# Kernel tuning notes

Measured on AMD Instinct MI355X. Metric: run time of the kernel, lower is better.

## Reference

```python
import jax, jax.numpy as jnp
from jax import lax
import numpy as np

T_NO = 50       # history / kernel half-length (hard-coded in module)
T_MAX = 101     # basis kernel length = 2*T_NO + 1
BASIS_NO = 34
HIST_BASIS_NO = 18
SIGMA = 3.0
HID = 20
SUB = 20


def _make_basis(n_basis, length):
    # basis[i, t] = exp(-(t - 3*i)^2 / sigma)
    raw = jnp.arange(length, dtype=jnp.float32)
    pts = 3.0 * jnp.arange(n_basis, dtype=jnp.float32)
    return jnp.exp(-((raw[None, :] - pts[:, None]) ** 2) / SIGMA)


def _conv1d(x, kern, pad):
    # x: [1, Cin, T], kern: [Cout, Cin, K] -> [1, Cout, T'] (torch F.conv1d semantics, cross-correlation)
    return lax.conv_general_dilated(x, kern, window_strides=(1,), padding=[(pad, pad)],
                                    dimension_numbers=('NCH', 'OIH', 'NCH'))


def setup_inputs() -> dict:
    key = jax.random.key(0)
    ks = jax.random.split(key, 12)
    T, Ee, Ei = 200000, 500, 100
    S_e = (jax.random.uniform(ks[0], (T, Ee)) < 0.05).astype(jnp.float32)
    S_i = (jax.random.uniform(ks[1], (T, Ei)) < 0.05).astype(jnp.float32)
    # one-hot synapse->subunit connectivity, as in the original model
    C_syn_e = jax.nn.one_hot(jax.random.randint(ks[2], (Ee,), 0, SUB), SUB, dtype=jnp.float32).T
    C_syn_i = jax.nn.one_hot(jax.random.randint(ks[3], (Ei,), 0, SUB), SUB, dtype=jnp.float32).T
    weight1 = 0.01 * jax.random.normal(ks[4], (HID, 2 * SUB, BASIS_NO), dtype=jnp.float32)
    weight4 = 0.01 * jax.random.normal(ks[5], (1, HID, BASIS_NO), dtype=jnp.float32)
    W_hist = 0.01 * jax.random.normal(ks[6], (HIST_BASIS_NO,), dtype=jnp.float32)
    Theta = 0.01 * jax.random.normal(ks[7], (1,), dtype=jnp.float32)
    W_spk = jnp.ones((1,), jnp.float32)
    Tau_spk = 3.0 * jnp.ones((1,), jnp.float32)
    u = jax.random.uniform(ks[8], (T,), dtype=jnp.float32)  # bernoulli noise
    return dict(S_e=S_e, S_i=S_i, C_syn_e=C_syn_e, C_syn_i=C_syn_i,
                weight1=weight1, weight4=weight4, W_hist=W_hist, Theta=Theta,
                W_spk=W_spk, Tau_spk=Tau_spk, u=u)


def reference(S_e, S_i, C_syn_e, C_syn_i, weight1, weight4, W_hist, Theta, W_spk, Tau_spk, u):
    basis = _make_basis(BASIS_NO, T_MAX)          # [34, 101]
    hist_basis = _make_basis(HIST_BASIS_NO, T_NO)  # [18, 50]

    kern1 = jnp.einsum('hsb,bt->hst', weight1, basis)  # [HID, 2*SUB, 101]
    kern4 = jnp.einsum('ohb,bt->oht', weight4, basis)  # [1, HID, 101]

    # route synapses to subunits, stack e/i: [1, 2*SUB, T]
    syn_in = jnp.concatenate([S_e @ C_syn_e.T, S_i @ C_syn_i.T], axis=1).T[None]
    out1 = jax.nn.leaky_relu(_conv1d(syn_in, kern1, T_NO), 0.01)  # [1, HID, T]
    out4 = _conv1d(out1, kern4, T_NO)[0, 0]                        # [T]

    hist_kern = W_hist @ hist_basis  # [50]
    theta = Theta[0]

    def step(buf, inp):
        # buf: last T_NO spikes, oldest first (== spk_out[t:t+T_NO])
        o_t, u_t = inp
        p = jax.nn.sigmoid(o_t + buf @ hist_kern + theta)
        spk = (u_t < p).astype(jnp.float32)  # torch.bernoulli(p)
        buf = jnp.concatenate([buf[1:], spk[None]])
        return buf, (p, spk)

    buf0 = jnp.zeros((T_NO,), jnp.float32)
    _, (prob_out, spikes) = lax.scan(step, buf0, (out4, u))
    spk_out = jnp.concatenate([jnp.zeros((T_NO,), jnp.float32), spikes])  # [T + T_NO]

    t = jnp.arange(T_NO, dtype=jnp.float32)
    t_tau = t / (Tau_spk[0] ** 2)
    spk_kern = t_tau * jnp.exp(-t_tau) * (W_spk[0] ** 2)  # unflipped; torch flips then cross-correlates
    # torch conv1d(x, flip(k), valid) == jnp.convolve(x, k, 'valid')
    spk_filt = jnp.convolve(spk_out, spk_kern, mode='valid')[:-1]  # [T]
    return (spk_filt, prob_out)
```

## Files before the change

kernel.cpp:

```cpp
#include <hip/hip_runtime.h>
#include <math.h>

#define T_TOT  200000
#define EE     500
#define EI     100
#define SUBN   20
#define NCH    40
#define HIDN   20
#define BNO    34
#define TM     101
#define TNO    50
#define HBNO   18
#define TT1    256
#define EPSF   2e-5f
#define NTAP   58
#define CPT    12

#define PADL   64
#define PADR   256
#define SROW   (PADL + T_TOT + PADR)

#define GROW   (T_TOT + 112)

#define GW     355
#define SW     380
#define CW     (2 * NTAP * CPT)

#define RTILE  512
#define RHALO  64
#define RRND   4
#define NT2    ((T_TOT + RTILE - 1) / RTILE)

__global__ void k_setup(const float* __restrict__ Ce, const float* __restrict__ Ci,
                        const float* __restrict__ Wh, const float* __restrict__ Wspk,
                        const float* __restrict__ Tau,
                        int* __restrict__ ae, int* __restrict__ ai,
                        float* __restrict__ hkpos, float* __restrict__ hkneg,
                        float* __restrict__ spkk, float* __restrict__ gtap,
                        double* __restrict__ hkd, double* __restrict__ basisd)
{
    int tid = threadIdx.x;
    if (tid < EE) {
        int a = 0;
        for (int s = 0; s < SUBN; ++s) if (Ce[s * EE + tid] > 0.5f) a = s;
        ae[tid] = a;
    } else if (tid < EE + EI) {
        int e = tid - EE; int a = 0;
        for (int s = 0; s < SUBN; ++s) if (Ci[s * EI + e] > 0.5f) a = s;
        ai[e] = a;
    } else if (tid < 664) {
        int j = tid - 600;
        double hk = 0.0;
        if (j >= 1 && j <= TNO) {
            int i = TNO - j;
            for (int b = 0; b < HBNO; ++b) {
                double d = (double)i - 3.0 * (double)b;
                hk += (double)Wh[b] * exp(-d * d / 3.0);
            }
        }
        hkd[j] = hk;
        hkpos[j] = (float)fmax(hk, 0.0);
        hkneg[j] = (float)fmin(hk, 0.0);
    } else if (tid < 728) {
        int m = tid - 664; float v = 0.f;
        if (m < TNO) {
            double tau2 = (double)Tau[0] * (double)Tau[0];
            double tt = (double)m / tau2;
            v = (float)(tt * exp(-tt) * (double)Wspk[0] * (double)Wspk[0]);
        }
        spkk[m] = v;
    } else if (tid < 753) {
        int j = tid - 740;
        gtap[tid - 728] = (float)exp(-(double)(j * j) / 3.0);
    }
    for (int idx = tid; idx < BNO * TM; idx += blockDim.x) {
        int b = idx / TM, k = idx % TM;
        double d = (double)k - 3.0 * (double)b;
        basisd[idx] = exp(-d * d / 3.0);
    }
}

__global__ void k_prep(const float* __restrict__ w1, const float* __restrict__ w4,
                       const double* __restrict__ basisd,
                       float* __restrict__ kern4, float* __restrict__ cmerged,
                       float* __restrict__ syn)
{
    int idx = blockIdx.x * 256 + threadIdx.x;
    if (idx < HIDN * TM) {
        int h = idx % HIDN, k = idx / HIDN;
        double acc = 0.0;
        for (int b = 0; b < BNO; ++b) acc += (double)w4[h * BNO + b] * basisd[b * TM + k];
        kern4[k * HIDN + h] = (float)acc;
    } else if (idx < 2020 + NCH * CW) {
        int j = idx - 2020;
        int f = j % CPT, tap = (j / CPT) % NTAP, hg = (j / (CPT * NTAP)) & 1, s = j / CW;
        float val = 0.f;
        if (f < 10) {
            int h = hg * 10 + f;
            if (tap < BNO) {
                val = w1[(h * NCH + s) * BNO + tap];
            } else {
                int mi = tap - BNO;
                int m = (mi < 12) ? (mi - 62) : (mi + 39);
                double acc = 0.0;
                for (int b = 0; b < BNO; ++b) {
                    int jj = m + 50 - 3 * b;
                    if (jj >= -12 && jj <= 12)
                        acc += (double)w1[(h * NCH + s) * BNO + b] * exp(-(double)(jj * jj) / 3.0);
                }
                val = -(float)acc;
            }
        }
        cmerged[j] = val;
    } else if (idx < 2020 + NCH * CW + NCH * (PADL + PADR)) {
        int j = idx - (2020 + NCH * CW);
        int r = j / (PADL + PADR), c = j % (PADL + PADR);
        int off = (c < PADL) ? c : (PADL + T_TOT + (c - PADL));
        syn[(size_t)r * SROW + off] = 0.f;
    }
}

__global__ __launch_bounds__(256) void k_route(const float* __restrict__ Se,
                                               const float* __restrict__ Si,
                                               const int* __restrict__ ae,
                                               const int* __restrict__ ai,
                                               float* __restrict__ syn)
{
    __shared__ float acc[NCH * 64];
    __shared__ int sae[EE];
    __shared__ int sai[EI];
    int tid = threadIdx.x;
    for (int i = tid; i < NCH * 64; i += 256) acc[i] = 0.f;
    for (int i = tid; i < EE; i += 256) sae[i] = ae[i];
    for (int i = tid; i < EI; i += 256) sai[i] = ai[i];
    __syncthreads();
    int t0 = blockIdx.x * 64;
    int lane = tid & 63, grp = tid >> 6;
    for (int ec = 0; ec < 2; ++ec) {
        int ev = ec * 64 + lane;
        if (ev < EE / 4) {
            int e = 4 * ev;
            int a0 = sae[e], a1 = sae[e + 1], a2 = sae[e + 2], a3 = sae[e + 3];
            for (int ts = grp; ts < 64; ts += 8) {
                float4 v1 = *(const float4*)(Se + (size_t)(t0 + ts) * EE + e);
                float4 v2 = *(const float4*)(Se + (size_t)(t0 + ts + 4) * EE + e);
                if (v1.x != 0.f) atomicAdd(&acc[a0 * 64 + ts], v1.x);
                if (v1.y != 0.f) atomicAdd(&acc[a1 * 64 + ts], v1.y);
                if (v1.z != 0.f) atomicAdd(&acc[a2 * 64 + ts], v1.z);
                if (v1.w != 0.f) atomicAdd(&acc[a3 * 64 + ts], v1.w);
                if (v2.x != 0.f) atomicAdd(&acc[a0 * 64 + ts + 4], v2.x);
                if (v2.y != 0.f) atomicAdd(&acc[a1 * 64 + ts + 4], v2.y);
                if (v2.z != 0.f) atomicAdd(&acc[a2 * 64 + ts + 4], v2.z);
                if (v2.w != 0.f) atomicAdd(&acc[a3 * 64 + ts + 4], v2.w);
            }
        }
    }
    {
        int ev = lane;
        if (ev < EI / 4) {
            int e = 4 * ev;
            int a0 = sai[e] + SUBN, a1 = sai[e + 1] + SUBN, a2 = sai[e + 2] + SUBN, a3 = sai[e + 3] + SUBN;
            for (int ts = grp; ts < 64; ts += 8) {
                float4 v1 = *(const float4*)(Si + (size_t)(t0 + ts) * EI + e);
                float4 v2 = *(const float4*)(Si + (size_t)(t0 + ts + 4) * EI + e);
                if (v1.x != 0.f) atomicAdd(&acc[a0 * 64 + ts], v1.x);
                if (v1.y != 0.f) atomicAdd(&acc[a1 * 64 + ts], v1.y);
                if (v1.z != 0.f) atomicAdd(&acc[a2 * 64 + ts], v1.z);
                if (v1.w != 0.f) atomicAdd(&acc[a3 * 64 + ts], v1.w);
                if (v2.x != 0.f) atomicAdd(&acc[a0 * 64 + ts + 4], v2.x);
                if (v2.y != 0.f) atomicAdd(&acc[a1 * 64 + ts + 4], v2.y);
                if (v2.z != 0.f) atomicAdd(&acc[a2 * 64 + ts + 4], v2.z);
                if (v2.w != 0.f) atomicAdd(&acc[a3 * 64 + ts + 4], v2.w);
            }
        }
    }
    __syncthreads();
    for (int i = tid; i < NCH * 64; i += 256) {
        int s = i >> 6, ts = i & 63;
        syn[(size_t)s * SROW + PADL + t0 + ts] = acc[i];
    }
}

__global__ __launch_bounds__(256) void k_prefilt(const float* __restrict__ syn,
                                                 const float* __restrict__ gtap,
                                                 float* __restrict__ G)
{
    int gi = blockIdx.x * 256 + threadIdx.x;
    if (gi >= GROW) return;
    const float* sp = syn + (size_t)blockIdx.y * SROW + PADL + (gi - 50);
    double a = 0.0;
#pragma unroll
    for (int j = -12; j <= 12; ++j)
        a += (double)gtap[j + 12] * (double)sp[j];
    G[(size_t)blockIdx.y * GROW + gi] = (float)a;
}

#define FMA10(c0, c1, c2, v0, v1)                                              \
    acc[0][0] = fmaf(c0.x, v0, acc[0][0]); acc[0][1] = fmaf(c0.x, v1, acc[0][1]); \
    acc[1][0] = fmaf(c0.y, v0, acc[1][0]); acc[1][1] = fmaf(c0.y, v1, acc[1][1]); \
    acc[2][0] = fmaf(c0.z, v0, acc[2][0]); acc[2][1] = fmaf(c0.z, v1, acc[2][1]); \
    acc[3][0] = fmaf(c0.w, v0, acc[3][0]); acc[3][1] = fmaf(c0.w, v1, acc[3][1]); \
    acc[4][0] = fmaf(c1.x, v0, acc[4][0]); acc[4][1] = fmaf(c1.x, v1, acc[4][1]); \
    acc[5][0] = fmaf(c1.y, v0, acc[5][0]); acc[5][1] = fmaf(c1.y, v1, acc[5][1]); \
    acc[6][0] = fmaf(c1.z, v0, acc[6][0]); acc[6][1] = fmaf(c1.z, v1, acc[6][1]); \
    acc[7][0] = fmaf(c1.w, v0, acc[7][0]); acc[7][1] = fmaf(c1.w, v1, acc[7][1]); \
    acc[8][0] = fmaf(c2.x, v0, acc[8][0]); acc[8][1] = fmaf(c2.x, v1, acc[8][1]); \
    acc[9][0] = fmaf(c2.y, v0, acc[9][0]); acc[9][1] = fmaf(c2.y, v1, acc[9][1]);

__global__ __launch_bounds__(256) void k_conv1w(const float* __restrict__ G,
                                                const float* __restrict__ syn,
                                                const float* __restrict__ cmerged,
                                                float* __restrict__ out1)
{
    __shared__ float sg[2][GW];
    __shared__ float ss[2][SW];
    __shared__ float sc[2][CW];
    int tid = threadIdx.x;
    int wv = tid >> 6, lane = tid & 63;
    int hg = wv & 1, tsub = wv >> 1;
    int tloc = tsub * 128 + lane * 2;
    int t0 = blockIdx.x * 256;

    {
        const float* Gp = G + t0;
        const float* sp = syn + PADL + t0 - 62;
        for (int i = tid; i < GW; i += 256) sg[0][i] = (t0 + i < GROW) ? Gp[i] : 0.f;
        for (int i = tid; i < SW; i += 256) ss[0][i] = sp[i];
        for (int i = tid; i < CW; i += 256) sc[0][i] = cmerged[i];
    }

    float acc[10][2];
#pragma unroll
    for (int hh = 0; hh < 10; ++hh) { acc[hh][0] = 0.f; acc[hh][1] = 0.f; }

    for (int s = 0; s < NCH; ++s) {
        __syncthreads();
        int cb = s & 1, nb = cb ^ 1;
        if (s + 1 < NCH) {
            const float* Gp = G + (size_t)(s + 1) * GROW + t0;
            const float* sp = syn + (size_t)(s + 1) * SROW + PADL + t0 - 62;
            const float* cp = cmerged + (size_t)(s + 1) * CW;
            for (int i = tid; i < GW; i += 256) sg[nb][i] = (t0 + i < GROW) ? Gp[i] : 0.f;
            for (int i = tid; i < SW; i += 256) ss[nb][i] = sp[i];
            for (int i = tid; i < CW; i += 256) sc[nb][i] = cp[i];
        }
        const float* sgc = sg[cb] + tloc;
        const float* ssc = ss[cb] + tloc;
        const float* cc = sc[cb] + hg * (NTAP * CPT);
#pragma unroll 2
        for (int b = 0; b < BNO; ++b) {
            float v0 = sgc[3 * b], v1 = sgc[3 * b + 1];
            const float* cp = cc + b * CPT;
            float4 c0 = *(const float4*)cp;
            float4 c1 = *(const float4*)(cp + 4);
            float2 c2 = *(const float2*)(cp + 8);
            FMA10(c0, c1, c2, v0, v1)
        }
#pragma unroll 2
        for (int mi = 0; mi < 12; ++mi) {
            float v0 = ssc[mi], v1 = ssc[mi + 1];
            const float* cp = cc + (BNO + mi) * CPT;
            float4 c0 = *(const float4*)cp;
            float4 c1 = *(const float4*)(cp + 4);
            float2 c2 = *(const float2*)(cp + 8);
            FMA10(c0, c1, c2, v0, v1)
        }
#pragma unroll 2
        for (int mi = 12; mi < 24; ++mi) {
            float v0 = ssc[mi + 101], v1 = ssc[mi + 102];
            const float* cp = cc + (BNO + mi) * CPT;
            float4 c0 = *(const float4*)cp;
            float4 c1 = *(const float4*)(cp + 4);
            float2 c2 = *(const float2*)(cp + 8);
            FMA10(c0, c1, c2, v0, v1)
        }
    }
    int t = t0 + tloc;
    if (t < T_TOT) {
#pragma unroll
        for (int hh = 0; hh < 10; ++hh) {
            float o0 = acc[hh][0], o1 = acc[hh][1];
            float2 st;
            st.x = (o0 > 0.f) ? o0 : 0.01f * o0;
            st.y = (o1 > 0.f) ? o1 : 0.01f * o1;
            *(float2*)(out1 + (size_t)(hg * 10 + hh) * T_TOT + t) = st;
        }
    }
}

__global__ __launch_bounds__(256) void k_conv2(const float* __restrict__ out1,
                                               const float* __restrict__ kern4,
                                               const float* __restrict__ Theta,
                                               const float* __restrict__ u,
                                               double* __restrict__ xd,
                                               double* __restrict__ thrd,
                                               float* __restrict__ thr32,
                                               float* __restrict__ blo,
                                               float* __restrict__ bhi)
{
    __shared__ float s1[HIDN * (TT1 + 100)];
    int tid = threadIdx.x;
    int t0 = blockIdx.x * TT1;
    for (int i = tid; i < HIDN * (TT1 + 100); i += 256) {
        int h = i / (TT1 + 100), x = i % (TT1 + 100);
        int g = t0 + x - TNO;
        s1[i] = (g >= 0 && g < T_TOT) ? out1[(size_t)h * T_TOT + g] : 0.f;
    }
    __syncthreads();
    int t = t0 + tid;
    if (t >= T_TOT) return;
    double acc = 0.0;
    for (int k = 0; k < TM; ++k) {
        const float* kp = kern4 + k * HIDN;
#pragma unroll
        for (int h = 0; h < HIDN; ++h)
            acc = fma((double)s1[h * (TT1 + 100) + tid + k], (double)kp[h], acc);
    }
    double x = acc + (double)Theta[0];
    double uu = (double)u[t];
    double th = (log(uu) - log1p(-uu)) - x;
    xd[t] = x; thrd[t] = th; thr32[t] = (float)th;
    blo[t + TNO] = 0.f;
    bhi[t + TNO] = 1.f;
    if (t < TNO) { blo[t] = 0.f; bhi[t] = 0.f; }
    if (t < 14)  { blo[T_TOT + TNO + t] = 0.f; bhi[T_TOT + TNO + t] = 0.f; }
}

__global__ __launch_bounds__(256) void k_relax(const float* __restrict__ thr32,
                                               const float* __restrict__ hkpos,
                                               const float* __restrict__ hkneg,
                                               float* __restrict__ blo,
                                               float* __restrict__ bhi,
                                               int wd, int* __restrict__ dirty)
{
    __shared__ float slo[RTILE + RHALO], shi[RTILE + RHALO];
    __shared__ float sth[RTILE + RHALO];
    __shared__ float shp[64], shn[64];
    int tid = threadIdx.x;
    int t0 = blockIdx.x * RTILE;
    for (int i = tid; i < RTILE + RHALO; i += 256) {
        int t = t0 - RHALO + i;
        int g = t + TNO;
        bool ok = (g >= 0 && g < T_TOT + 64);
        slo[i] = ok ? blo[g] : 0.f;
        shi[i] = ok ? bhi[g] : 0.f;
        sth[i] = (t >= 0 && t < T_TOT) ? thr32[t] : 0.f;
    }
    if (tid < 64) { shp[tid] = hkpos[tid]; shn[tid] = hkneg[tid]; }
    __syncthreads();
    for (int r = 0; r < RRND; ++r) {
        for (int i = tid; i < RTILE + RHALO; i += 256) {
            if (i < TNO) continue;
            float l = slo[i], h = shi[i];
            if (l == h) continue;
            float lo = 0.f, hi = 0.f;
            for (int j = 1; j <= TNO; ++j) {
                float bl = slo[i - j], bh = shi[i - j];
                float hp = shp[j], hn = shn[j];
                lo = fmaf(hp, bl, lo); lo = fmaf(hn, bh, lo);
                hi = fmaf(hp, bh, hi); hi = fmaf(hn, bl, hi);
            }
            float th = sth[i];
            if (lo > th + EPSF)      slo[i] = 1.f;
            else if (hi < th - EPSF) shi[i] = 0.f;
        }
        __syncthreads();
    }
    for (int i = tid; i < RTILE; i += 256) {
        int t = t0 + i;
        if (t < T_TOT) {
            blo[t + TNO] = slo[RHALO + i];
            bhi[t + TNO] = shi[RHALO + i];
        }
    }
    if (wd) {
        int i1 = tid, i2 = tid + 256;
        int u1 = (t0 + i1 < T_TOT) && (slo[RHALO + i1] != shi[RHALO + i1]);
        int u2 = (t0 + i2 < T_TOT) && (slo[RHALO + i2] != shi[RHALO + i2]);
        int c = __syncthreads_count(u1);
        c += __syncthreads_count(u2);
        if (tid == 0) dirty[blockIdx.x] = c;
    }
}

__global__ __launch_bounds__(512) void k_compact(const float* __restrict__ blo,
                                                 const float* __restrict__ bhi,
                                                 const int* __restrict__ dirty,
                                                 int* __restrict__ list,
                                                 int* __restrict__ utot)
{
    __shared__ int wsum[8];
    __shared__ int sd[NT2];
    __shared__ int sbase;
    int tid = threadIdx.x;
    for (int i = tid; i < NT2; i += 512) sd[i] = dirty[i];
    int t = blockIdx.x * 512 + tid;
    int unk = (t < T_TOT) && (blo[t + TNO] != bhi[t + TNO]);
    unsigned long long m = __ballot(unk);
    int lane = tid & 63, wv = tid >> 6;
    int lr = __popcll(m & ((1ull << lane) - 1ull));
    if (lane == 0) wsum[wv] = __popcll(m);
    __syncthreads();
    if (tid == 0) {
        int b = 0;
        for (int k = 0; k < (int)blockIdx.x; ++k) b += sd[k];
        sbase = b;
        if (blockIdx.x == 0) {
            int tot = 0;
            for (int k = 0; k < NT2; ++k) tot += sd[k];
            utot[0] = tot;
        }
        int r = 0;
        for (int k = 0; k < 8; ++k) { int c = wsum[k]; wsum[k] = r; r += c; }
    }
    __syncthreads();
    if (unk) list[sbase + wsum[wv] + lr] = t;
}

__global__ __launch_bounds__(256) void k_afix(const int* __restrict__ list,
                                              const int* __restrict__ utot,
                                              const float* __restrict__ blo,
                                              const double* __restrict__ hkd,
                                              double* __restrict__ afix)
{
    int i = blockIdx.x * 256 + threadIdx.x;
    if (i >= utot[0]) return;
    int t = list[i];
    double a = 0.0;
    for (int j = 1; j <= TNO; ++j)
        a += hkd[j] * (double)blo[t - j + TNO];
    afix[i] = a;
}

__global__ __launch_bounds__(256) void k_chain(const int* __restrict__ list,
                                               int* __restrict__ utot,
                                               int* __restrict__ chead)
{
    __shared__ int wcnt[4];
    __shared__ int base_s;
    int tid = threadIdx.x, lane = tid & 63, wv = tid >> 6;
    int U = utot[0];
    if (tid == 0) base_s = 0;
    __syncthreads();
    for (int b0 = 0; b0 < U; b0 += 256) {
        int i = b0 + tid;
        int head = 0;
        if (i < U) head = (i == 0) || (list[i] - list[i - 1] > TNO);
        unsigned long long m = __ballot(head);
        int pre = __popcll(m & ((1ull << lane) - 1ull));
        if (lane == 0) wcnt[wv] = __popcll(m);
        __syncthreads();
        int wbase = 0;
        for (int k = 0; k < wv; ++k) wbase += wcnt[k];
        int tot = wcnt[0] + wcnt[1] + wcnt[2] + wcnt[3];
        if (head) chead[base_s + wbase + pre] = i;
        __syncthreads();
        if (tid == 0) base_s += tot;
        __syncthreads();
    }
    if (tid == 0) utot[1] = base_s;
}

__global__ __launch_bounds__(256) void k_cresolve(const int* __restrict__ list,
                                                  const int* __restrict__ chead,
                                                  const double* __restrict__ afix,
                                                  const double* __restrict__ thrd,
                                                  const double* __restrict__ hkd,
                                                  const int* __restrict__ utot,
                                                  int* bits,
                                                  float* __restrict__ blo,
                                                  float* __restrict__ bhi)
{
    __shared__ double shk[64];
    if (threadIdx.x < 64)
        shk[threadIdx.x] = (threadIdx.x >= 1 && threadIdx.x <= TNO) ? hkd[threadIdx.x] : 0.0;
    __syncthreads();
    int c = blockIdx.x * 256 + threadIdx.x;
    int nch = utot[1];
    if (c >= nch) return;
    int i0 = chead[c];
    int i1 = (c + 1 < nch) ? chead[c + 1] : utot[0];
    for (int i = i0; i < i1; ++i) {
        int t = list[i];
        double a = afix[i];
        for (int k = i - 1; k >= i0; --k) {
            int dt = t - list[k];
            if (dt > TNO) break;
            if (bits[k]) a += shk[dt];
        }
        int sb = (a > thrd[t]) ? 1 : 0;
        bits[i] = sb;
        float f = (float)sb;
        blo[t + TNO] = f;
        bhi[t + TNO] = f;
    }
}

__global__ __launch_bounds__(256) void k_out(const float* __restrict__ blo,
                                             const float* __restrict__ spkk,
                                             const double* __restrict__ hkd,
                                             const double* __restrict__ xd,
                                             float* __restrict__ outp)
{
    __shared__ float sb[TT1 + 64];
    __shared__ float ssp[64];
    __shared__ double shk[64];
    int tid = threadIdx.x;
    int t0 = blockIdx.x * TT1;
    for (int i = tid; i < TT1 + TNO; i += 256) {
        int g = t0 + i;
        sb[i] = (g < T_TOT + 64) ? blo[g] : 0.f;
    }
    if (tid < 64) { ssp[tid] = spkk[tid]; shk[tid] = hkd[tid]; }
    __syncthreads();
    int t = t0 + tid;
    if (t >= T_TOT) return;
    float filt = 0.f;
    double a = 0.0;
    for (int m = 1; m <= TNO; ++m) {
        float b = sb[tid + TNO - m];
        filt = fmaf(b, ssp[m - 1], filt);
        a += shk[m] * (double)b;
    }
    double p = 1.0 / (1.0 + exp(-(xd[t] + a)));
    outp[t] = filt;
    outp[T_TOT + t] = (float)p;
}

extern "C" void kernel_launch(void* const* d_in, const int* in_sizes, int n_in,
                              void* d_out, int out_size, void* d_ws, size_t ws_size,
                              hipStream_t stream)
{
    (void)in_sizes; (void)n_in; (void)out_size; (void)ws_size;
    const float* Se = (const float*)d_in[0];
    const float* Si = (const float*)d_in[1];
    const float* Ce = (const float*)d_in[2];
    const float* Ci = (const float*)d_in[3];
    const float* w1 = (const float*)d_in[4];
    const float* w4 = (const float*)d_in[5];
    const float* Wh = (const float*)d_in[6];
    const float* Th = (const float*)d_in[7];
    const float* Ws = (const float*)d_in[8];
    const float* Ta = (const float*)d_in[9];
    const float* u  = (const float*)d_in[10];

    char* w = (char*)d_ws;
    size_t off = 0;
    auto alloc = [&](size_t n) { size_t o = off; off += (n + 15) & ~(size_t)15; return o; };

    size_t gzone = alloc((size_t)NCH * GROW * 4);
    float*  G     = (float*)(w + gzone);
    double* xd    = (double*)(w + gzone);
    double* thrd  = (double*)(w + gzone + 1600000);
    float*  thr32 = (float*)(w + gzone + 3200000);
    float*  blo   = (float*)(w + gzone + 4000000);
    float*  bhi   = (float*)(w + gzone + 4800512);
    int*    dirty = (int*)(w + gzone + 5601024);
    int*    utot  = (int*)(w + gzone + 5603072);
    int*    list  = (int*)(w + gzone + 5603200);
    double* afix  = (double*)(w + gzone + 6403200);
    int*    chead = (int*)(w + gzone + 8003200);
    int*    bits  = (int*)(w + gzone + 8803216);

    float*  syn     = (float*)(w + alloc((size_t)NCH * SROW * 4));
    float*  out1    = (float*)(w + alloc((size_t)HIDN * T_TOT * 4));
    float*  kern4   = (float*)(w + alloc((size_t)TM * HIDN * 4));
    float*  cmerged = (float*)(w + alloc((size_t)NCH * CW * 4));
    double* basisd  = (double*)(w + alloc((size_t)BNO * TM * 8));
    int*    ae      = (int*)(w + alloc(EE * 4));
    int*    ai      = (int*)(w + alloc(EI * 4));
    float*  hkpos   = (float*)(w + alloc(64 * 4));
    float*  hkneg   = (float*)(w + alloc(64 * 4));
    float*  spkk    = (float*)(w + alloc(64 * 4));
    float*  gtap    = (float*)(w + alloc(32 * 4));
    double* hkd     = (double*)(w + alloc(64 * 8));

    k_setup<<<1, 1024, 0, stream>>>(Ce, Ci, Wh, Ws, Ta, ae, ai, hkpos, hkneg, spkk, gtap, hkd, basisd);
    int prepN = 2020 + NCH * CW + NCH * (PADL + PADR);
    k_prep<<<(prepN + 255) / 256, 256, 0, stream>>>(w1, w4, basisd, kern4, cmerged, syn);
    k_route<<<T_TOT / 64, 256, 0, stream>>>(Se, Si, ae, ai, syn);
    dim3 pg((GROW + 255) / 256, NCH);
    k_prefilt<<<pg, 256, 0, stream>>>(syn, gtap, G);
    k_conv1w<<<(T_TOT + 255) / 256, 256, 0, stream>>>(G, syn, cmerged, out1);
    k_conv2<<<(T_TOT + TT1 - 1) / TT1, 256, 0, stream>>>(out1, kern4, Th, u, xd, thrd, thr32, blo, bhi);
    k_relax<<<NT2, 256, 0, stream>>>(thr32, hkpos, hkneg, blo, bhi, 0, dirty);
    k_relax<<<NT2, 256, 0, stream>>>(thr32, hkpos, hkneg, blo, bhi, 1, dirty);
    k_compact<<<NT2, 512, 0, stream>>>(blo, bhi, dirty, list, utot);
    k_chain<<<1, 256, 0, stream>>>(list, utot, chead);
    k_afix<<<(T_TOT + 255) / 256, 256, 0, stream>>>(list, utot, blo, hkd, afix);
    k_cresolve<<<(T_TOT + 255) / 256, 256, 0, stream>>>(list, chead, afix, thrd, hkd, utot, bits, blo, bhi);
    k_out<<<(T_TOT + TT1 - 1) / TT1, 256, 0, stream>>>(blo, spkk, hkd, xd, (float*)d_out);
}
```

Before: 1.133 ms.

## Read conv weights from global memory, interleave time mapping, fuse resolve kernels

The conv1 kernel stops staging the merged weights in shared memory and reads them directly from global memory with a wave-uniform hidden-group index, so the loads can become scalar. Each lane now covers two time points 64 apart instead of two adjacent ones, and the unroll factor rises to 4. Separately, the afix computation is folded into the compaction kernel, and chain-head discovery plus chain resolution are merged into one 1024-thread single-block kernel, which removes two launches. The risk is that resolving all chains inside a single block serializes work that previously ran across many blocks.

```diff
diff --git a/kernel.cpp b/kernel.cpp
--- a/kernel.cpp
+++ b/kernel.cpp
@@ -214,11 +214,11 @@
 {
     __shared__ float sg[2][GW];
     __shared__ float ss[2][SW];
-    __shared__ float sc[2][CW];
     int tid = threadIdx.x;
     int wv = tid >> 6, lane = tid & 63;
-    int hg = wv & 1, tsub = wv >> 1;
-    int tloc = tsub * 128 + lane * 2;
+    int hg = __builtin_amdgcn_readfirstlane(wv & 1);
+    int tsub = wv >> 1;
+    int tloc = tsub * 128 + lane;
     int t0 = blockIdx.x * 256;
 
     {
@@ -226,7 +226,6 @@
         const float* sp = syn + PADL + t0 - 62;
         for (int i = tid; i < GW; i += 256) sg[0][i] = (t0 + i < GROW) ? Gp[i] : 0.f;
         for (int i = tid; i < SW; i += 256) ss[0][i] = sp[i];
-        for (int i = tid; i < CW; i += 256) sc[0][i] = cmerged[i];
     }
 
     float acc[10][2];
@@ -239,35 +238,33 @@
         if (s + 1 < NCH) {
             const float* Gp = G + (size_t)(s + 1) * GROW + t0;
             const float* sp = syn + (size_t)(s + 1) * SROW + PADL + t0 - 62;
-            const float* cp = cmerged + (size_t)(s + 1) * CW;
             for (int i = tid; i < GW; i += 256) sg[nb][i] = (t0 + i < GROW) ? Gp[i] : 0.f;
             for (int i = tid; i < SW; i += 256) ss[nb][i] = sp[i];
-            for (int i = tid; i < CW; i += 256) sc[nb][i] = cp[i];
         }
         const float* sgc = sg[cb] + tloc;
         const float* ssc = ss[cb] + tloc;
-        const float* cc = sc[cb] + hg * (NTAP * CPT);
-#pragma unroll 2
+        const float* cc = cmerged + (size_t)s * CW + hg * (NTAP * CPT);
+#pragma unroll 4
         for (int b = 0; b < BNO; ++b) {
-            float v0 = sgc[3 * b], v1 = sgc[3 * b + 1];
+            float v0 = sgc[3 * b], v1 = sgc[3 * b + 64];
             const float* cp = cc + b * CPT;
             float4 c0 = *(const float4*)cp;
             float4 c1 = *(const float4*)(cp + 4);
             float2 c2 = *(const float2*)(cp + 8);
             FMA10(c0, c1, c2, v0, v1)
         }
-#pragma unroll 2
+#pragma unroll 4
         for (int mi = 0; mi < 12; ++mi) {
-            float v0 = ssc[mi], v1 = ssc[mi + 1];
+            float v0 = ssc[mi], v1 = ssc[mi + 64];
             const float* cp = cc + (BNO + mi) * CPT;
             float4 c0 = *(const float4*)cp;
             float4 c1 = *(const float4*)(cp + 4);
             float2 c2 = *(const float2*)(cp + 8);
             FMA10(c0, c1, c2, v0, v1)
         }
-#pragma unroll 2
+#pragma unroll 4
         for (int mi = 12; mi < 24; ++mi) {
-            float v0 = ssc[mi + 101], v1 = ssc[mi + 102];
+            float v0 = ssc[mi + 101], v1 = ssc[mi + 165];
             const float* cp = cc + (BNO + mi) * CPT;
             float4 c0 = *(const float4*)cp;
             float4 c1 = *(const float4*)(cp + 4);
@@ -275,16 +272,13 @@
             FMA10(c0, c1, c2, v0, v1)
         }
     }
-    int t = t0 + tloc;
-    if (t < T_TOT) {
+    int t1 = t0 + tloc, t2 = t1 + 64;
 #pragma unroll
-        for (int hh = 0; hh < 10; ++hh) {
-            float o0 = acc[hh][0], o1 = acc[hh][1];
-            float2 st;
-            st.x = (o0 > 0.f) ? o0 : 0.01f * o0;
-            st.y = (o1 > 0.f) ? o1 : 0.01f * o1;
-            *(float2*)(out1 + (size_t)(hg * 10 + hh) * T_TOT + t) = st;
-        }
+    for (int hh = 0; hh < 10; ++hh) {
+        int h = hg * 10 + hh;
+        float o0 = acc[hh][0], o1 = acc[hh][1];
+        if (t1 < T_TOT) out1[(size_t)h * T_TOT + t1] = (o0 > 0.f) ? o0 : 0.01f * o0;
+        if (t2 < T_TOT) out1[(size_t)h * T_TOT + t2] = (o1 > 0.f) ? o1 : 0.01f * o1;
     }
 }
 
@@ -386,8 +380,10 @@
 __global__ __launch_bounds__(512) void k_compact(const float* __restrict__ blo,
                                                  const float* __restrict__ bhi,
                                                  const int* __restrict__ dirty,
+                                                 const double* __restrict__ hkd,
                                                  int* __restrict__ list,
-                                                 int* __restrict__ utot)
+                                                 int* __restrict__ utot,
+                                                 double* __restrict__ afix)
 {
     __shared__ int wsum[8];
     __shared__ int sd[NT2];
@@ -414,35 +410,35 @@
         for (int k = 0; k < 8; ++k) { int c = wsum[k]; wsum[k] = r; r += c; }
     }
     __syncthreads();
-    if (unk) list[sbase + wsum[wv] + lr] = t;
-}
-
-__global__ __launch_bounds__(256) void k_afix(const int* __restrict__ list,
-                                              const int* __restrict__ utot,
-                                              const float* __restrict__ blo,
-                                              const double* __restrict__ hkd,
-                                              double* __restrict__ afix)
-{
-    int i = blockIdx.x * 256 + threadIdx.x;
-    if (i >= utot[0]) return;
-    int t = list[i];
-    double a = 0.0;
-    for (int j = 1; j <= TNO; ++j)
-        a += hkd[j] * (double)blo[t - j + TNO];
-    afix[i] = a;
-}
-
-__global__ __launch_bounds__(256) void k_chain(const int* __restrict__ list,
-                                               int* __restrict__ utot,
-                                               int* __restrict__ chead)
-{
-    __shared__ int wcnt[4];
+    if (unk) {
+        int pos = sbase + wsum[wv] + lr;
+        list[pos] = t;
+        double a = 0.0;
+        for (int j = 1; j <= TNO; ++j)
+            a += hkd[j] * (double)blo[t - j + TNO];
+        afix[pos] = a;
+    }
+}
+
+__global__ __launch_bounds__(1024) void k_chainres(const int* __restrict__ list,
+                                                   const double* __restrict__ afix,
+                                                   const double* __restrict__ thrd,
+                                                   const double* __restrict__ hkd,
+                                                   const int* __restrict__ utot,
+                                                   int* __restrict__ chead,
+                                                   int* __restrict__ bits,
+                                                   float* __restrict__ blo,
+                                                   float* __restrict__ bhi)
+{
+    __shared__ double shk[64];
+    __shared__ int wcnt[16];
     __shared__ int base_s;
     int tid = threadIdx.x, lane = tid & 63, wv = tid >> 6;
+    if (tid < 64) shk[tid] = (tid >= 1 && tid <= TNO) ? hkd[tid] : 0.0;
+    if (tid == 0) base_s = 0;
     int U = utot[0];
-    if (tid == 0) base_s = 0;
-    __syncthreads();
-    for (int b0 = 0; b0 < U; b0 += 256) {
+    __syncthreads();
+    for (int b0 = 0; b0 < U; b0 += 1024) {
         int i = b0 + tid;
         int head = 0;
         if (i < U) head = (i == 0) || (list[i] - list[i - 1] > TNO);
@@ -452,47 +448,31 @@
         __syncthreads();
         int wbase = 0;
         for (int k = 0; k < wv; ++k) wbase += wcnt[k];
-        int tot = wcnt[0] + wcnt[1] + wcnt[2] + wcnt[3];
+        int tot = 0;
+        for (int k = 0; k < 16; ++k) tot += wcnt[k];
         if (head) chead[base_s + wbase + pre] = i;
         __syncthreads();
         if (tid == 0) base_s += tot;
         __syncthreads();
     }
-    if (tid == 0) utot[1] = base_s;
-}
-
-__global__ __launch_bounds__(256) void k_cresolve(const int* __restrict__ list,
-                                                  const int* __restrict__ chead,
-                                                  const double* __restrict__ afix,
-                                                  const double* __restrict__ thrd,
-                                                  const double* __restrict__ hkd,
-                                                  const int* __restrict__ utot,
-                                                  int* bits,
-                                                  float* __restrict__ blo,
-                                                  float* __restrict__ bhi)
-{
-    __shared__ double shk[64];
-    if (threadIdx.x < 64)
-        shk[threadIdx.x] = (threadIdx.x >= 1 && threadIdx.x <= TNO) ? hkd[threadIdx.x] : 0.0;
-    __syncthreads();
-    int c = blockIdx.x * 256 + threadIdx.x;
-    int nch = utot[1];
-    if (c >= nch) return;
-    int i0 = chead[c];
-    int i1 = (c + 1 < nch) ? chead[c + 1] : utot[0];
-    for (int i = i0; i < i1; ++i) {
-        int t = list[i];
-        double a = afix[i];
-        for (int k = i - 1; k >= i0; --k) {
-            int dt = t - list[k];
-            if (dt > TNO) break;
-            if (bits[k]) a += shk[dt];
-        }
-        int sb = (a > thrd[t]) ? 1 : 0;
-        bits[i] = sb;
-        float f = (float)sb;
-        blo[t + TNO] = f;
-        bhi[t + TNO] = f;
+    int nch = base_s;
+    for (int c = tid; c < nch; c += 1024) {
+        int i0 = chead[c];
+        int i1 = (c + 1 < nch) ? chead[c + 1] : U;
+        for (int i = i0; i < i1; ++i) {
+            int t = list[i];
+            double a = afix[i];
+            for (int k = i - 1; k >= i0; --k) {
+                int dt = t - list[k];
+                if (dt > TNO) break;
+                if (bits[k]) a += shk[dt];
+            }
+            int sb = (a > thrd[t]) ? 1 : 0;
+            bits[i] = sb;
+            float f = (float)sb;
+            blo[t + TNO] = f;
+            bhi[t + TNO] = f;
+        }
     }
 }
 
@@ -585,9 +565,7 @@
     k_conv2<<<(T_TOT + TT1 - 1) / TT1, 256, 0, stream>>>(out1, kern4, Th, u, xd, thrd, thr32, blo, bhi);
     k_relax<<<NT2, 256, 0, stream>>>(thr32, hkpos, hkneg, blo, bhi, 0, dirty);
     k_relax<<<NT2, 256, 0, stream>>>(thr32, hkpos, hkneg, blo, bhi, 1, dirty);
-    k_compact<<<NT2, 512, 0, stream>>>(blo, bhi, dirty, list, utot);
-    k_chain<<<1, 256, 0, stream>>>(list, utot, chead);
-    k_afix<<<(T_TOT + 255) / 256, 256, 0, stream>>>(list, utot, blo, hkd, afix);
-    k_cresolve<<<(T_TOT + 255) / 256, 256, 0, stream>>>(list, chead, afix, thrd, hkd, utot, bits, blo, bhi);
+    k_compact<<<NT2, 512, 0, stream>>>(blo, bhi, dirty, hkd, list, utot, afix);
+    k_chainres<<<1, 1024, 0, stream>>>(list, afix, thrd, hkd, utot, chead, bits, blo, bhi);
     k_out<<<(T_TOT + TT1 - 1) / TT1, 256, 0, stream>>>(blo, spkk, hkd, xd, (float*)d_out);
 }
```

Measured after the change: 1.213 ms. 7.1% more time.
